# Kernel optimization log

Hardware: AMD Instinct MI355X
Metric: run time of the kernel (lower is better)

Reference implementation:

```python
import jax, jax.numpy as jnp
import numpy as np

B, T, D, H = 2, 1024, 1024, 16
HS = D // H
EPS = 1e-5
SCALE = float(np.sqrt(HS))  # faithful bug: scores / hs**(-0.5) == scores * sqrt(hs)


def setup_inputs() -> dict:
    key = jax.random.key(0)
    ks = jax.random.split(key, 20)
    n = lambda k, shape: jax.random.normal(k, shape, dtype=jnp.float32) * 0.02
    return {
        "src": jax.random.normal(ks[0], (B, T, D), dtype=jnp.float32),
        "att": jax.random.normal(ks[1], (B, T, D), dtype=jnp.float32),
        # causal masked self-attention (no biases on q/k/v)
        "wq_m": n(ks[2], (H, D, HS)), "wk_m": n(ks[3], (H, D, HS)), "wv_m": n(ks[4], (H, D, HS)),
        "proj_m_w": n(ks[5], (D, D)), "proj_m_b": jnp.zeros((D,), jnp.float32),
        # final (cross) attention (biases on q/k/v)
        "wq_f": n(ks[6], (H, D, HS)), "wk_f": n(ks[7], (H, D, HS)), "wv_f": n(ks[8], (H, D, HS)),
        "bq_f": jnp.zeros((H, HS), jnp.float32), "bk_f": jnp.zeros((H, HS), jnp.float32),
        "bv_f": jnp.zeros((H, HS), jnp.float32),
        "proj_f_w": n(ks[9], (D, D)), "proj_f_b": jnp.zeros((D,), jnp.float32),
        # FFN
        "w1": n(ks[10], (D, 4 * D)), "b1": jnp.zeros((4 * D,), jnp.float32),
        "w2": n(ks[11], (4 * D, D)), "b2": jnp.zeros((D,), jnp.float32),
        # shared RMSNorm weight (one instance reused at all three sites)
        "norm_w": jnp.ones((D,), jnp.float32),
    }


def rmsnorm(x, w):
    return x * jax.lax.rsqrt(jnp.mean(x * x, axis=-1, keepdims=True) + EPS) * w


def masked_attn(x, wq, wk, wv):
    q = jnp.einsum('btd,hde->bhte', x, wq)
    k = jnp.einsum('btd,hde->bhte', x, wk)
    v = jnp.einsum('btd,hde->bhte', x, wv)
    scores = jnp.einsum('bhte,bhse->bhts', q, k) * SCALE  # [B,H,T,T]
    causal = jnp.tril(jnp.ones((T, T), dtype=bool))
    scores = jnp.where(causal, scores, -jnp.inf)
    a = jax.nn.softmax(scores, axis=-1)
    o = jnp.einsum('bhts,bhse->bhte', a, v)
    return o.transpose(0, 2, 1, 3).reshape(B, T, D)  # concat heads


def final_attn(x, att, wq, bq, wk, bk, wv, bv):
    q = jnp.einsum('btd,hde->bhte', att, wq) + bq[None, :, None, :]
    k = jnp.einsum('btd,hde->bhte', att, wk) + bk[None, :, None, :]
    v = jnp.einsum('btd,hde->bhte', x, wv) + bv[None, :, None, :]
    scores = jnp.einsum('bhte,bhse->bhts', q, k) * SCALE
    a = jax.nn.softmax(scores, axis=-1)
    o = jnp.einsum('bhts,bhse->bhte', a, v)
    return o.transpose(0, 2, 1, 3).reshape(B, T, D)


def reference(src, att, wq_m, wk_m, wv_m, proj_m_w, proj_m_b,
              wq_f, wk_f, wv_f, bq_f, bk_f, bv_f, proj_f_w, proj_f_b,
              w1, b1, w2, b2, norm_w):
    # masked self-attention block
    m = masked_attn(rmsnorm(src, norm_w), wq_m, wk_m, wv_m)
    m_out = src + (m @ proj_m_w + proj_m_b)
    # cross attention block (q/k from norm(att), v from m_out)
    f = final_attn(m_out, rmsnorm(att, norm_w), wq_f, bq_f, wk_f, bk_f, wv_f, bv_f)
    f_out = m_out + (f @ proj_f_w + proj_f_b)
    # FFN block
    h = rmsnorm(f_out, norm_w)
    h = jax.nn.gelu(h @ w1 + b1, approximate=False) @ w2 + b2
    return f_out + h
```

## Files before the change

### kernel.cpp

```cpp
#include <hip/hip_runtime.h>
#include <math.h>

#define BB 2
#define TT 1024
#define DD 1024
#define HH 16
#define HS 64
#define NROWS (BB*TT)

typedef _Float16 f16;
typedef __attribute__((ext_vector_type(8))) _Float16 half8;
typedef __attribute__((ext_vector_type(4))) _Float16 half4;
typedef __attribute__((ext_vector_type(4))) float f32x4;

constexpr float EPS   = 1e-5f;
constexpr float SCALE = 8.0f;

__device__ __forceinline__ void load_lds16(const f16* g, f16* l) {
    __builtin_amdgcn_global_load_lds(
        (const __attribute__((address_space(1))) unsigned int*)g,
        (__attribute__((address_space(3))) unsigned int*)l, 16, 0, 0);
}

__device__ __forceinline__ int xcd_swizzle(int lin, int total) {
    if ((total & 7) == 0) {
        const int chunk = total >> 3;
        lin = (lin & 7) * chunk + (lin >> 3);
    }
    return lin;
}

__global__ __launch_bounds__(256) void rmsnorm_kernel(const float* __restrict__ x,
                                                      const float* __restrict__ w,
                                                      f16* __restrict__ out) {
    const int row = blockIdx.x;
    const int tid = threadIdx.x;
    const float* xr = x + (size_t)row * DD;

    float4 xv = reinterpret_cast<const float4*>(xr)[tid];
    float ss = xv.x*xv.x + xv.y*xv.y + xv.z*xv.z + xv.w*xv.w;

    __shared__ float red[256];
    red[tid] = ss; __syncthreads();
    for (int s = 128; s > 0; s >>= 1) {
        if (tid < s) red[tid] += red[tid + s];
        __syncthreads();
    }
    const float inv = rsqrtf(red[0] * (1.0f / DD) + EPS);

    float4 wv = reinterpret_cast<const float4*>(w)[tid];
    half4 o;
    o.x = (f16)(xv.x * inv * wv.x);
    o.y = (f16)(xv.y * inv * wv.y);
    o.z = (f16)(xv.z * inv * wv.z);
    o.w = (f16)(xv.w * inv * wv.w);
    *reinterpret_cast<half4*>(&out[(size_t)row * DD + tid * 4]) = o;
}

__global__ __launch_bounds__(256) void wtrans_all(
    const float* __restrict__ wq_m, const float* __restrict__ wk_m,
    const float* __restrict__ wv_m, const float* __restrict__ proj_m_w,
    const float* __restrict__ wq_f, const float* __restrict__ wk_f,
    const float* __restrict__ wv_f, const float* __restrict__ proj_f_w,
    const float* __restrict__ w1,   const float* __restrict__ w2,
    f16* __restrict__ d_qkvm, f16* __restrict__ d_projm,
    f16* __restrict__ d_qkvf, f16* __restrict__ d_projf,
    f16* __restrict__ d_w1,   f16* __restrict__ d_w2,
    const float* __restrict__ bq, const float* __restrict__ bk,
    const float* __restrict__ bv, float* __restrict__ biascat)
{
    const int bid = blockIdx.x;
    const int tid = threadIdx.x;
    const size_t M_ = 1024 * 1024;

    if (bid >= 4096) {
        #pragma unroll
        for (int r = 0; r < 4; ++r) {
            const int j = r * 256 + tid;
            biascat[j] = bq[j]; biascat[j + 1024] = bk[j]; biascat[j + 2048] = bv[j];
        }
        return;
    }

    const float* W; f16* Wt; int K, N, lognk, t; bool headw;
    if (bid < 768)       { const int m = bid >> 8;
                           W = (m == 0) ? wq_m : (m == 1) ? wk_m : wv_m;
                           Wt = d_qkvm + (size_t)m * M_;
                           K = 1024; N = 1024; lognk = 4; headw = true;  t = bid & 255; }
    else if (bid < 1024) { W = proj_m_w; Wt = d_projm;
                           K = 1024; N = 1024; lognk = 4; headw = false; t = bid - 768; }
    else if (bid < 1792) { const int m = (bid - 1024) >> 8;
                           W = (m == 0) ? wq_f : (m == 1) ? wk_f : wv_f;
                           Wt = d_qkvf + (size_t)m * M_;
                           K = 1024; N = 1024; lognk = 4; headw = true;  t = (bid - 1024) & 255; }
    else if (bid < 2048) { W = proj_f_w; Wt = d_projf;
                           K = 1024; N = 1024; lognk = 4; headw = false; t = bid - 1792; }
    else if (bid < 3072) { W = w1; Wt = d_w1;
                           K = 1024; N = 4096; lognk = 4; headw = false; t = bid - 2048; }
    else                 { W = w2; Wt = d_w2;
                           K = 4096; N = 1024; lognk = 6; headw = false; t = bid - 3072; }

    const int k0 = (t & ((1 << lognk) - 1)) * 64;
    const int n0 = (t >> lognk) * 64;

    __shared__ float tt[64][65];
    #pragma unroll
    for (int r = 0; r < 4; ++r) {
        const int idx = tid + r * 256;
        const int kl  = idx >> 4;
        const int nl4 = (idx & 15) * 4;
        const float* gp;
        if (headw) {
            gp = W + ((size_t)(n0 >> 6) * K + (k0 + kl)) * 64 + nl4;
        } else {
            gp = W + (size_t)(k0 + kl) * N + n0 + nl4;
        }
        float4 v = *reinterpret_cast<const float4*>(gp);
        tt[kl][nl4 + 0] = v.x; tt[kl][nl4 + 1] = v.y;
        tt[kl][nl4 + 2] = v.z; tt[kl][nl4 + 3] = v.w;
    }
    __syncthreads();
    #pragma unroll
    for (int r = 0; r < 4; ++r) {
        const int idx = tid + r * 256;
        const int nl  = idx >> 4;
        const int kl4 = (idx & 15) * 4;
        half4 o;
        o.x = (f16)tt[kl4 + 0][nl];
        o.y = (f16)tt[kl4 + 1][nl];
        o.z = (f16)tt[kl4 + 2][nl];
        o.w = (f16)tt[kl4 + 3][nl];
        *reinterpret_cast<half4*>(&Wt[(size_t)(n0 + nl) * K + k0 + kl4]) = o;
    }
}

template<int BM, int EPI, bool HEADOUT, bool SPLITA, bool OHALF, bool OUT2, bool PARTIAL>
__global__ __launch_bounds__(256, 2) void gemm_mfma(
    const f16* __restrict__ A1,
    const f16* __restrict__ A2,
    const f16* __restrict__ Bt,
    const float* __restrict__ bias,
    const float* __restrict__ resid,
    float* __restrict__ outF,
    f16* __restrict__ outH,
    f16* __restrict__ outH2,
    int N, int K, int splitN)
{
    constexpr int BK = 32;
    constexpr int MI = 4;
    constexpr int NI = (BM == 128) ? 4 : 2;
    constexpr int WN = (BM == 128) ? 64 : 32;
    constexpr int ASLOT = BM * 4;
    constexpr int AINST = ASLOT / 256;

    __shared__ f16 ldsA[2][ASLOT * 8];
    __shared__ f16 ldsB[2][512 * 8];

    const int tid  = threadIdx.x;
    const int lane = tid & 63;
    const int wid  = tid >> 6;
    const int gy = gridDim.y;
    const int lin = xcd_swizzle(blockIdx.y * gridDim.x + blockIdx.x,
                                gridDim.x * gy);
    const int m0 = (lin % gy) * BM;
    const int n0 = (lin / gy) * 128;
    const int wm = (BM == 128) ? (wid >> 1) : 0;
    const int wn = (BM == 128) ? (wid & 1) : wid;

    const int Klen  = K / gridDim.z;
    const int kbase = blockIdx.z * Klen;

    const f16* Aptr = (SPLITA && n0 >= splitN) ? A2 : A1;

    f32x4 acc[MI][NI];
    #pragma unroll
    for (int i = 0; i < MI; ++i)
        #pragma unroll
        for (int j = 0; j < NI; ++j)
            acc[i][j] = (f32x4){0.f, 0.f, 0.f, 0.f};

    auto stage = [&](int buf, int kt) {
        const int k0 = kbase + kt * BK;
        #pragma unroll
        for (int i = 0; i < AINST; ++i) {
            const int s   = (wid * AINST + i) * 64 + lane;
            const int kh  = s / BM;
            const int row = s % BM;
            load_lds16(Aptr + (size_t)(m0 + row) * K + (k0 + kh * 8),
                       &ldsA[buf][s * 8]);
        }
        #pragma unroll
        for (int i = 0; i < 2; ++i) {
            const int s   = (wid * 2 + i) * 64 + lane;
            const int kh  = s >> 7;
            const int col = s & 127;
            load_lds16(Bt + (size_t)(n0 + col) * K + (k0 + kh * 8),
                       &ldsB[buf][s * 8]);
        }
    };

    const int NT = Klen / BK;
    stage(0, 0);
    __syncthreads();
    int cur = 0;
    const int l15 = lane & 15, l4 = lane >> 4;
    for (int kt = 0; kt < NT; ++kt) {
        if (kt + 1 < NT) stage(cur ^ 1, kt + 1);
        half8 af[MI], bfr[NI];
        #pragma unroll
        for (int mi = 0; mi < MI; ++mi)
            af[mi] = *reinterpret_cast<const half8*>(
                &ldsA[cur][(l4 * BM + wm * 64 + mi * 16 + l15) * 8]);
        #pragma unroll
        for (int ni = 0; ni < NI; ++ni)
            bfr[ni] = *reinterpret_cast<const half8*>(
                &ldsB[cur][(l4 * 128 + wn * WN + ni * 16 + l15) * 8]);
        #pragma unroll
        for (int mi = 0; mi < MI; ++mi)
            #pragma unroll
            for (int ni = 0; ni < NI; ++ni)
                acc[mi][ni] = __builtin_amdgcn_mfma_f32_16x16x32_f16(
                    af[mi], bfr[ni], acc[mi][ni], 0, 0, 0);
        __syncthreads();
        cur ^= 1;
    }

    float* pout = nullptr;
    if (PARTIAL) {
        const size_t MN = (size_t)gridDim.y * BM * N;
        pout = outF + (size_t)blockIdx.z * MN;
    }

    #pragma unroll
    for (int mi = 0; mi < MI; ++mi) {
        #pragma unroll
        for (int ni = 0; ni < NI; ++ni) {
            #pragma unroll
            for (int r = 0; r < 4; ++r) {
                const int row = m0 + wm * 64 + mi * 16 + l4 * 4 + r;
                const int col = n0 + wn * WN + ni * 16 + l15;
                float v = acc[mi][ni][r];
                if (PARTIAL) {
                    pout[(size_t)row * N + col] = v;
                    continue;
                }
                if (EPI >= 1) v += bias[col];
                if (EPI == 2) v = 0.5f * v * (1.0f + erff(v * 0.70710678118f));
                if (EPI == 3) v += resid[(size_t)row * N + col];
                size_t oidx;
                if (HEADOUT) {
                    const int mat = col >> 10;
                    const int h = (col >> 6) & 15, e = col & 63;
                    const int b = row >> 10, t = row & (TT - 1);
                    oidx = (size_t)mat * ((size_t)NROWS * DD)
                         + ((size_t)((b * HH + h) * TT + t)) * HS + e;
                } else {
                    oidx = (size_t)row * N + col;
                }
                if (OHALF) outH[oidx] = (f16)v;
                else       outF[oidx] = v;
                if (OUT2)  outH2[oidx] = (f16)v;
            }
        }
    }
}

template<bool OUT2>
__global__ __launch_bounds__(256) void reduce4(const float* __restrict__ part,
                                               const float* __restrict__ bias,
                                               const float* __restrict__ resid,
                                               float* __restrict__ outF,
                                               f16* __restrict__ outH2,
                                               int N) {
    const size_t MN  = (size_t)gridDim.x * 1024;
    const size_t idx = ((size_t)blockIdx.x * 256 + threadIdx.x) * 4;
    float4 a = *reinterpret_cast<const float4*>(part + idx);
    float4 b = *reinterpret_cast<const float4*>(part + MN + idx);
    float4 c = *reinterpret_cast<const float4*>(part + 2 * MN + idx);
    float4 d = *reinterpret_cast<const float4*>(part + 3 * MN + idx);
    float4 bi = *reinterpret_cast<const float4*>(bias + (idx & (size_t)(N - 1)));
    float4 rs = *reinterpret_cast<const float4*>(resid + idx);
    float4 o;
    o.x = a.x + b.x + c.x + d.x + bi.x + rs.x;
    o.y = a.y + b.y + c.y + d.y + bi.y + rs.y;
    o.z = a.z + b.z + c.z + d.z + bi.z + rs.z;
    o.w = a.w + b.w + c.w + d.w + bi.w + rs.w;
    *reinterpret_cast<float4*>(outF + idx) = o;
    if (OUT2) {
        half4 h;
        h.x = (f16)o.x; h.y = (f16)o.y; h.z = (f16)o.z; h.w = (f16)o.w;
        *reinterpret_cast<half4*>(outH2 + idx) = h;
    }
}

template<bool CAUSAL>
__global__ __launch_bounds__(256) void attn_mfma(const f16* __restrict__ Q,
                                                 const f16* __restrict__ Kg,
                                                 const f16* __restrict__ Vg,
                                                 f16* __restrict__ O) {
    const int iq  = blockIdx.x;
    const int bh  = blockIdx.y;
    const int tid = threadIdx.x;
    const int lane = tid & 63;
    const int w   = tid >> 6;
    const int l15 = lane & 15, l4 = lane >> 4;

    __shared__ f16 Ks[512 * 8];
    __shared__ f16 VT[64 * 72];
    __shared__ f16 Ps[4][16 * 72];

    const f16* qb = Q  + ((size_t)bh * TT + (size_t)iq * 64) * HS;
    const f16* kb = Kg + (size_t)bh * TT * HS;
    const f16* vb = Vg + (size_t)bh * TT * HS;

    half8 qf[2];
    #pragma unroll
    for (int ks = 0; ks < 2; ++ks)
        qf[ks] = *reinterpret_cast<const half8*>(
            qb + (size_t)(w * 16 + l15) * HS + ks * 32 + l4 * 8);

    f32x4 oacc[4];
    #pragma unroll
    for (int ni = 0; ni < 4; ++ni) oacc[ni] = (f32x4){0.f, 0.f, 0.f, 0.f};
    float m_run[4], l_run[4];
    #pragma unroll
    for (int r = 0; r < 4; ++r) { m_run[r] = -1e30f; l_run[r] = 0.f; }

    const int sp  = lane & 31;
    const int ehv = lane >> 5;
    const int c0  = w * 16 + ehv * 8;

    const int ntiles = CAUSAL ? (iq + 1) : (TT / 64);
    for (int js = 0; js < ntiles; ++js) {
        __syncthreads();

        #pragma unroll
        for (int i = 0; i < 2; ++i) {
            const int slot = (w * 2 + i) * 64 + lane;
            load_lds16(kb + (size_t)(js * 64 + (slot & 63)) * HS + (slot >> 6) * 8,
                       &Ks[slot * 8]);
        }
        {
            const f16* vrow = vb + (size_t)(js * 64 + 2 * sp) * HS + c0;
            uint4 r0 = *reinterpret_cast<const uint4*>(vrow);
            uint4 r1 = *reinterpret_cast<const uint4*>(vrow + HS);
            const unsigned rc0[4] = {r0.x, r0.y, r0.z, r0.w};
            const unsigned rc1[4] = {r1.x, r1.y, r1.z, r1.w};
            #pragma unroll
            for (int i = 0; i < 8; ++i) {
                const unsigned lo = (i & 1) ? (rc0[i >> 1] >> 16) : (rc0[i >> 1] & 0xffffu);
                const unsigned hi = (i & 1) ? (rc1[i >> 1] >> 16) : (rc1[i >> 1] & 0xffffu);
                *reinterpret_cast<unsigned*>(&VT[(c0 + i) * 72 + 2 * sp]) = lo | (hi << 16);
            }
        }
        __syncthreads();

        f32x4 sacc[4];
        #pragma unroll
        for (int ni = 0; ni < 4; ++ni) sacc[ni] = (f32x4){0.f, 0.f, 0.f, 0.f};
        #pragma unroll
        for (int ks = 0; ks < 2; ++ks) {
            #pragma unroll
            for (int ni = 0; ni < 4; ++ni) {
                half8 kf = *reinterpret_cast<const half8*>(
                    &Ks[((ks * 4 + l4) * 64 + ni * 16 + l15) * 8]);
                sacc[ni] = __builtin_amdgcn_mfma_f32_16x16x32_f16(qf[ks], kf, sacc[ni], 0, 0, 0);
            }
        }

        float sv[4][4];
        #pragma unroll
        for (int ni = 0; ni < 4; ++ni) {
            #pragma unroll
            for (int r = 0; r < 4; ++r) {
                float x = sacc[ni][r] * SCALE;
                if (CAUSAL && js == iq) {
                    const int sg = js * 64 + ni * 16 + l15;
                    const int qg = iq * 64 + w * 16 + l4 * 4 + r;
                    if (sg > qg) x = -1e30f;
                }
                sv[ni][r] = x;
            }
        }

        #pragma unroll
        for (int r = 0; r < 4; ++r) {
            float rm = fmaxf(fmaxf(sv[0][r], sv[1][r]), fmaxf(sv[2][r], sv[3][r]));
            rm = fmaxf(rm, __shfl_xor(rm, 1));
            rm = fmaxf(rm, __shfl_xor(rm, 2));
            rm = fmaxf(rm, __shfl_xor(rm, 4));
            rm = fmaxf(rm, __shfl_xor(rm, 8));
            const float mnew = fmaxf(m_run[r], rm);
            const float corr = __expf(m_run[r] - mnew);
            float p0 = __expf(sv[0][r] - mnew);
            float p1 = __expf(sv[1][r] - mnew);
            float p2 = __expf(sv[2][r] - mnew);
            float p3 = __expf(sv[3][r] - mnew);
            float sum = p0 + p1 + p2 + p3;
            sum += __shfl_xor(sum, 1);
            sum += __shfl_xor(sum, 2);
            sum += __shfl_xor(sum, 4);
            sum += __shfl_xor(sum, 8);
            l_run[r] = l_run[r] * corr + sum;
            m_run[r] = mnew;
            #pragma unroll
            for (int ni = 0; ni < 4; ++ni) oacc[ni][r] *= corr;
            f16* prow = &Ps[w][(l4 * 4 + r) * 72];
            prow[ 0 + l15] = (f16)p0;
            prow[16 + l15] = (f16)p1;
            prow[32 + l15] = (f16)p2;
            prow[48 + l15] = (f16)p3;
        }

        #pragma unroll
        for (int ks = 0; ks < 2; ++ks) {
            half8 pf = *reinterpret_cast<const half8*>(&Ps[w][l15 * 72 + ks * 32 + l4 * 8]);
            #pragma unroll
            for (int ni = 0; ni < 4; ++ni) {
                half8 vf = *reinterpret_cast<const half8*>(
                    &VT[(ni * 16 + l15) * 72 + ks * 32 + l4 * 8]);
                oacc[ni] = __builtin_amdgcn_mfma_f32_16x16x32_f16(pf, vf, oacc[ni], 0, 0, 0);
            }
        }
    }

    const int b = bh >> 4, h = bh & (HH - 1);
    #pragma unroll
    for (int r = 0; r < 4; ++r) {
        const float inv = 1.0f / l_run[r];
        const int t = iq * 64 + w * 16 + l4 * 4 + r;
        #pragma unroll
        for (int ni = 0; ni < 4; ++ni)
            O[((size_t)(b * TT + t)) * DD + h * HS + ni * 16 + l15] =
                (f16)(oacc[ni][r] * inv);
    }
}

extern "C" void kernel_launch(void* const* d_in, const int* in_sizes, int n_in,
                              void* d_out, int out_size, void* d_ws, size_t ws_size,
                              hipStream_t stream) {
    const float* src      = (const float*)d_in[0];
    const float* att      = (const float*)d_in[1];
    const float* wq_m     = (const float*)d_in[2];
    const float* wk_m     = (const float*)d_in[3];
    const float* wv_m     = (const float*)d_in[4];
    const float* proj_m_w = (const float*)d_in[5];
    const float* proj_m_b = (const float*)d_in[6];
    const float* wq_f     = (const float*)d_in[7];
    const float* wk_f     = (const float*)d_in[8];
    const float* wv_f     = (const float*)d_in[9];
    const float* bq_f     = (const float*)d_in[10];
    const float* bk_f     = (const float*)d_in[11];
    const float* bv_f     = (const float*)d_in[12];
    const float* proj_f_w = (const float*)d_in[13];
    const float* proj_f_b = (const float*)d_in[14];
    const float* w1       = (const float*)d_in[15];
    const float* b1       = (const float*)d_in[16];
    const float* w2       = (const float*)d_in[17];
    const float* b2       = (const float*)d_in[18];
    const float* norm_w   = (const float*)d_in[19];

    const size_t M_ = 1024 * 1024;
    f16* wsb = (f16*)d_ws;
    f16* wt_qkvm = wsb;
    f16* wt_projm = wsb + 3 * M_;
    f16* wt_qkvf = wsb + 4 * M_;
    f16* wt_projf = wsb + 7 * M_;
    f16* wt_w1   = wsb + 8 * M_;
    f16* wt_w2   = wsb + 12 * M_;
    f16* xn  = wsb + 16 * M_;
    f16* qkv = wsb + 18 * M_;
    f16* ao  = wsb + 24 * M_;
    f16* h1  = wsb + 18 * M_;
    float* m_out = (float*)(wsb + 26 * M_);
    float* partb = (float*)(wsb + 30 * M_);
    f16* mo_h  = (f16*)d_out;
    float* biascat = (float*)((char*)d_out + 4 * 1024 * 1024);
    float* f_out = (float*)d_out;
    float* outp  = (float*)d_out;
    (void)ws_size; (void)in_sizes; (void)n_in;

    const dim3 blk(256);
    const int BIG = 1 << 30;
    const dim3 gQKV(24, 32);
    const dim3 gW1(32, 32);
    const dim3 gSPLIT(8, 32, 4);
    const dim3 gRED(2048);

    wtrans_all<<<dim3(4097), blk, 0, stream>>>(
        wq_m, wk_m, wv_m, proj_m_w, wq_f, wk_f, wv_f, proj_f_w, w1, w2,
        wt_qkvm, wt_projm, wt_qkvf, wt_projf, wt_w1, wt_w2,
        bq_f, bk_f, bv_f, biascat);

    rmsnorm_kernel<<<dim3(NROWS), blk, 0, stream>>>(src, norm_w, xn);
    gemm_mfma<64, 0, true, false, true, false, false><<<gQKV, blk, 0, stream>>>(
        xn, nullptr, wt_qkvm, nullptr, nullptr, nullptr, qkv, nullptr, 3072, 1024, BIG);
    attn_mfma<true><<<dim3(16, 32), blk, 0, stream>>>(qkv, qkv + 2 * M_, qkv + 4 * M_, ao);
    gemm_mfma<64, 0, false, false, false, false, true><<<gSPLIT, blk, 0, stream>>>(
        ao, nullptr, wt_projm, nullptr, nullptr, partb, nullptr, nullptr, 1024, 1024, BIG);
    reduce4<true><<<gRED, blk, 0, stream>>>(partb, proj_m_b, src, m_out, mo_h, 1024);

    rmsnorm_kernel<<<dim3(NROWS), blk, 0, stream>>>(att, norm_w, xn);
    gemm_mfma<64, 1, true, true, true, false, false><<<gQKV, blk, 0, stream>>>(
        xn, mo_h, wt_qkvf, biascat, nullptr, nullptr, qkv, nullptr, 3072, 1024, 2048);
    attn_mfma<false><<<dim3(16, 32), blk, 0, stream>>>(qkv, qkv + 2 * M_, qkv + 4 * M_, ao);
    gemm_mfma<64, 0, false, false, false, false, true><<<gSPLIT, blk, 0, stream>>>(
        ao, nullptr, wt_projf, nullptr, nullptr, partb, nullptr, nullptr, 1024, 1024, BIG);
    reduce4<false><<<gRED, blk, 0, stream>>>(partb, proj_f_b, m_out, f_out, nullptr, 1024);

    rmsnorm_kernel<<<dim3(NROWS), blk, 0, stream>>>(f_out, norm_w, xn);
    gemm_mfma<64, 2, false, false, true, false, false><<<gW1, blk, 0, stream>>>(
        xn, nullptr, wt_w1, b1, nullptr, nullptr, h1, nullptr, 4096, 1024, BIG);
    gemm_mfma<64, 0, false, false, false, false, true><<<gSPLIT, blk, 0, stream>>>(
        h1, nullptr, wt_w2, nullptr, nullptr, partb, nullptr, nullptr, 1024, 4096, BIG);
    reduce4<false><<<gRED, blk, 0, stream>>>(partb, b2, f_out, outp, nullptr, 1024);
}
```

Baseline: 364.5 us.

## Restructure pipeline: merge norms and QKV GEMMs, fp16 split-K partials, fused reduce-norm

Both RMSNorms (src and att) now run in one launch. The masked QKV and the cross-attention Q/K projections run as a single 5120-wide GEMM with BM=128, and only the V projection of m_out stays as a separate GEMM. Split-K partials are stored in fp16 instead of fp32, which halves partial-buffer traffic. The second reduction also fuses the final RMSNorm, which removes a launch. Risks are precision loss from the fp16 partials and the residual m_out now being kept only in fp16. BM=128 tiles may also reduce occupancy and CU fill for the smaller grids.

```diff
diff --git a/kernel.cpp b/kernel.cpp
--- a/kernel.cpp
+++ b/kernel.cpp
@@ -30,12 +30,16 @@
     return lin;
 }
 
-__global__ __launch_bounds__(256) void rmsnorm_kernel(const float* __restrict__ x,
-                                                      const float* __restrict__ w,
-                                                      f16* __restrict__ out) {
-    const int row = blockIdx.x;
+__global__ __launch_bounds__(256) void rms2_kernel(const float* __restrict__ src,
+                                                   const float* __restrict__ att,
+                                                   const float* __restrict__ w,
+                                                   f16* __restrict__ xn_s,
+                                                   f16* __restrict__ xn_a) {
+    const int bid = blockIdx.x;
     const int tid = threadIdx.x;
-    const float* xr = x + (size_t)row * DD;
+    const int row = bid & (NROWS - 1);
+    const float* xr = ((bid < NROWS) ? src : att) + (size_t)row * DD;
+    f16* out = ((bid < NROWS) ? xn_s : xn_a) + (size_t)row * DD;
 
     float4 xv = reinterpret_cast<const float4*>(xr)[tid];
     float ss = xv.x*xv.x + xv.y*xv.y + xv.z*xv.z + xv.w*xv.w;
@@ -54,7 +58,7 @@
     o.y = (f16)(xv.y * inv * wv.y);
     o.z = (f16)(xv.z * inv * wv.z);
     o.w = (f16)(xv.w * inv * wv.w);
-    *reinterpret_cast<half4*>(&out[(size_t)row * DD + tid * 4]) = o;
+    *reinterpret_cast<half4*>(&out[tid * 4]) = o;
 }
 
 __global__ __launch_bounds__(256) void wtrans_all(
@@ -63,41 +67,36 @@
     const float* __restrict__ wq_f, const float* __restrict__ wk_f,
     const float* __restrict__ wv_f, const float* __restrict__ proj_f_w,
     const float* __restrict__ w1,   const float* __restrict__ w2,
-    f16* __restrict__ d_qkvm, f16* __restrict__ d_projm,
-    f16* __restrict__ d_qkvf, f16* __restrict__ d_projf,
-    f16* __restrict__ d_w1,   f16* __restrict__ d_w2,
+    f16* __restrict__ wt,
     const float* __restrict__ bq, const float* __restrict__ bk,
-    const float* __restrict__ bv, float* __restrict__ biascat)
+    float* __restrict__ biascat)
 {
     const int bid = blockIdx.x;
     const int tid = threadIdx.x;
     const size_t M_ = 1024 * 1024;
 
     if (bid >= 4096) {
-        #pragma unroll
-        for (int r = 0; r < 4; ++r) {
-            const int j = r * 256 + tid;
-            biascat[j] = bq[j]; biascat[j + 1024] = bk[j]; biascat[j + 2048] = bv[j];
-        }
+        for (int j = tid; j < 5120; j += 256)
+            biascat[j] = (j < 3072) ? 0.f : ((j < 4096) ? bq[j - 3072] : bk[j - 4096]);
         return;
     }
 
     const float* W; f16* Wt; int K, N, lognk, t; bool headw;
     if (bid < 768)       { const int m = bid >> 8;
                            W = (m == 0) ? wq_m : (m == 1) ? wk_m : wv_m;
-                           Wt = d_qkvm + (size_t)m * M_;
+                           Wt = wt + (size_t)m * M_;
                            K = 1024; N = 1024; lognk = 4; headw = true;  t = bid & 255; }
-    else if (bid < 1024) { W = proj_m_w; Wt = d_projm;
+    else if (bid < 1024) { W = proj_m_w; Wt = wt + 6 * M_;
                            K = 1024; N = 1024; lognk = 4; headw = false; t = bid - 768; }
     else if (bid < 1792) { const int m = (bid - 1024) >> 8;
                            W = (m == 0) ? wq_f : (m == 1) ? wk_f : wv_f;
-                           Wt = d_qkvf + (size_t)m * M_;
+                           Wt = wt + (size_t)(3 + m) * M_;
                            K = 1024; N = 1024; lognk = 4; headw = true;  t = (bid - 1024) & 255; }
-    else if (bid < 2048) { W = proj_f_w; Wt = d_projf;
+    else if (bid < 2048) { W = proj_f_w; Wt = wt + 7 * M_;
                            K = 1024; N = 1024; lognk = 4; headw = false; t = bid - 1792; }
-    else if (bid < 3072) { W = w1; Wt = d_w1;
+    else if (bid < 3072) { W = w1; Wt = wt + 8 * M_;
                            K = 1024; N = 4096; lognk = 4; headw = false; t = bid - 2048; }
-    else                 { W = w2; Wt = d_w2;
+    else                 { W = w2; Wt = wt + 12 * M_;
                            K = 4096; N = 1024; lognk = 6; headw = false; t = bid - 3072; }
 
     const int k0 = (t & ((1 << lognk) - 1)) * 64;
@@ -134,16 +133,14 @@
     }
 }
 
-template<int BM, int EPI, bool HEADOUT, bool SPLITA, bool OHALF, bool OUT2, bool PARTIAL>
+template<int BM, int EPI, bool HEADOUT, bool SPLITA, bool OHALF, bool PARTIAL>
 __global__ __launch_bounds__(256, 2) void gemm_mfma(
     const f16* __restrict__ A1,
     const f16* __restrict__ A2,
     const f16* __restrict__ Bt,
     const float* __restrict__ bias,
-    const float* __restrict__ resid,
     float* __restrict__ outF,
     f16* __restrict__ outH,
-    f16* __restrict__ outH2,
     int N, int K, int splitN)
 {
     constexpr int BK = 32;
@@ -225,10 +222,10 @@
         cur ^= 1;
     }
 
-    float* pout = nullptr;
+    f16* pout = nullptr;
     if (PARTIAL) {
         const size_t MN = (size_t)gridDim.y * BM * N;
-        pout = outF + (size_t)blockIdx.z * MN;
+        pout = outH + (size_t)blockIdx.z * MN;
     }
 
     #pragma unroll
@@ -241,12 +238,11 @@
                 const int col = n0 + wn * WN + ni * 16 + l15;
                 float v = acc[mi][ni][r];
                 if (PARTIAL) {
-                    pout[(size_t)row * N + col] = v;
+                    pout[(size_t)row * N + col] = (f16)v;
                     continue;
                 }
                 if (EPI >= 1) v += bias[col];
                 if (EPI == 2) v = 0.5f * v * (1.0f + erff(v * 0.70710678118f));
-                if (EPI == 3) v += resid[(size_t)row * N + col];
                 size_t oidx;
                 if (HEADOUT) {
                     const int mat = col >> 10;
@@ -259,37 +255,69 @@
                 }
                 if (OHALF) outH[oidx] = (f16)v;
                 else       outF[oidx] = v;
-                if (OUT2)  outH2[oidx] = (f16)v;
             }
         }
     }
 }
 
-template<bool OUT2>
-__global__ __launch_bounds__(256) void reduce4(const float* __restrict__ part,
-                                               const float* __restrict__ bias,
-                                               const float* __restrict__ resid,
-                                               float* __restrict__ outF,
-                                               f16* __restrict__ outH2,
-                                               int N) {
-    const size_t MN  = (size_t)gridDim.x * 1024;
-    const size_t idx = ((size_t)blockIdx.x * 256 + threadIdx.x) * 4;
-    float4 a = *reinterpret_cast<const float4*>(part + idx);
-    float4 b = *reinterpret_cast<const float4*>(part + MN + idx);
-    float4 c = *reinterpret_cast<const float4*>(part + 2 * MN + idx);
-    float4 d = *reinterpret_cast<const float4*>(part + 3 * MN + idx);
-    float4 bi = *reinterpret_cast<const float4*>(bias + (idx & (size_t)(N - 1)));
-    float4 rs = *reinterpret_cast<const float4*>(resid + idx);
-    float4 o;
-    o.x = a.x + b.x + c.x + d.x + bi.x + rs.x;
-    o.y = a.y + b.y + c.y + d.y + bi.y + rs.y;
-    o.z = a.z + b.z + c.z + d.z + bi.z + rs.z;
-    o.w = a.w + b.w + c.w + d.w + bi.w + rs.w;
-    *reinterpret_cast<float4*>(outF + idx) = o;
-    if (OUT2) {
+template<int MODE>
+__global__ __launch_bounds__(256) void reduce_fuse(const f16* __restrict__ part,
+                                                   const float* __restrict__ bias,
+                                                   const float* __restrict__ residF,
+                                                   const f16* __restrict__ residH,
+                                                   float* __restrict__ outF,
+                                                   f16* __restrict__ outH,
+                                                   const float* __restrict__ normw,
+                                                   f16* __restrict__ xnout) {
+    const size_t MN  = (size_t)NROWS * 1024;
+    const int tid = threadIdx.x;
+    const size_t idx = ((size_t)blockIdx.x * 256 + tid) * 4;
+    float o[4];
+    {
+        half4 p0 = *reinterpret_cast<const half4*>(part + idx);
+        half4 p1 = *reinterpret_cast<const half4*>(part + MN + idx);
+        half4 p2 = *reinterpret_cast<const half4*>(part + 2 * MN + idx);
+        half4 p3 = *reinterpret_cast<const half4*>(part + 3 * MN + idx);
+        float4 bi = *reinterpret_cast<const float4*>(bias + (idx & 1023));
+        o[0] = (float)p0.x + (float)p1.x + (float)p2.x + (float)p3.x + bi.x;
+        o[1] = (float)p0.y + (float)p1.y + (float)p2.y + (float)p3.y + bi.y;
+        o[2] = (float)p0.z + (float)p1.z + (float)p2.z + (float)p3.z + bi.z;
+        o[3] = (float)p0.w + (float)p1.w + (float)p2.w + (float)p3.w + bi.w;
+    }
+    if (MODE == 0 || MODE == 2) {
+        float4 rs = *reinterpret_cast<const float4*>(residF + idx);
+        o[0] += rs.x; o[1] += rs.y; o[2] += rs.z; o[3] += rs.w;
+    } else {
+        half4 rh = *reinterpret_cast<const half4*>(residH + idx);
+        o[0] += (float)rh.x; o[1] += (float)rh.y; o[2] += (float)rh.z; o[3] += (float)rh.w;
+    }
+
+    if (MODE == 0) {
         half4 h;
-        h.x = (f16)o.x; h.y = (f16)o.y; h.z = (f16)o.z; h.w = (f16)o.w;
-        *reinterpret_cast<half4*>(outH2 + idx) = h;
+        h.x = (f16)o[0]; h.y = (f16)o[1]; h.z = (f16)o[2]; h.w = (f16)o[3];
+        *reinterpret_cast<half4*>(outH + idx) = h;
+        return;
+    }
+
+    float4 ov = {o[0], o[1], o[2], o[3]};
+    *reinterpret_cast<float4*>(outF + idx) = ov;
+
+    if (MODE == 1) {
+        __shared__ float red[256];
+        red[tid] = o[0]*o[0] + o[1]*o[1] + o[2]*o[2] + o[3]*o[3];
+        __syncthreads();
+        for (int s = 128; s > 0; s >>= 1) {
+            if (tid < s) red[tid] += red[tid + s];
+            __syncthreads();
+        }
+        const float inv = rsqrtf(red[0] * (1.0f / DD) + EPS);
+        float4 nw = *reinterpret_cast<const float4*>(normw + (idx & 1023));
+        half4 h;
+        h.x = (f16)(o[0] * inv * nw.x);
+        h.y = (f16)(o[1] * inv * nw.y);
+        h.z = (f16)(o[2] * inv * nw.z);
+        h.w = (f16)(o[3] * inv * nw.w);
+        *reinterpret_cast<half4*>(xnout + idx) = h;
     }
 }
 
@@ -462,56 +490,55 @@
 
     const size_t M_ = 1024 * 1024;
     f16* wsb = (f16*)d_ws;
-    f16* wt_qkvm = wsb;
-    f16* wt_projm = wsb + 3 * M_;
-    f16* wt_qkvf = wsb + 4 * M_;
-    f16* wt_projf = wsb + 7 * M_;
-    f16* wt_w1   = wsb + 8 * M_;
-    f16* wt_w2   = wsb + 12 * M_;
-    f16* xn  = wsb + 16 * M_;
-    f16* qkv = wsb + 18 * M_;
-    f16* ao  = wsb + 24 * M_;
-    f16* h1  = wsb + 18 * M_;
-    float* m_out = (float*)(wsb + 26 * M_);
-    float* partb = (float*)(wsb + 30 * M_);
-    f16* mo_h  = (f16*)d_out;
-    float* biascat = (float*)((char*)d_out + 4 * 1024 * 1024);
+    f16* wt      = wsb;
+    f16* headbuf = wsb + 16 * M_;
+    f16* h1      = wsb + 16 * M_;
+    f16* xn_s    = wsb + 28 * M_;
+    f16* xn_a    = wsb + 30 * M_;
+    f16* ao      = wsb + 32 * M_;
+    f16* mo_h    = wsb + 34 * M_;
+    f16* partH   = wsb + 36 * M_;
+    float* biascat = (float*)d_out;
     float* f_out = (float*)d_out;
     float* outp  = (float*)d_out;
     (void)ws_size; (void)in_sizes; (void)n_in;
 
     const dim3 blk(256);
     const int BIG = 1 << 30;
-    const dim3 gQKV(24, 32);
-    const dim3 gW1(32, 32);
-    const dim3 gSPLIT(8, 32, 4);
+    const dim3 gQKV(40, 16);
+    const dim3 gVF(8, 32);
+    const dim3 gW1(32, 16);
+    const dim3 gSPLIT(8, 16, 4);
     const dim3 gRED(2048);
 
     wtrans_all<<<dim3(4097), blk, 0, stream>>>(
         wq_m, wk_m, wv_m, proj_m_w, wq_f, wk_f, wv_f, proj_f_w, w1, w2,
-        wt_qkvm, wt_projm, wt_qkvf, wt_projf, wt_w1, wt_w2,
-        bq_f, bk_f, bv_f, biascat);
-
-    rmsnorm_kernel<<<dim3(NROWS), blk, 0, stream>>>(src, norm_w, xn);
-    gemm_mfma<64, 0, true, false, true, false, false><<<gQKV, blk, 0, stream>>>(
-        xn, nullptr, wt_qkvm, nullptr, nullptr, nullptr, qkv, nullptr, 3072, 1024, BIG);
-    attn_mfma<true><<<dim3(16, 32), blk, 0, stream>>>(qkv, qkv + 2 * M_, qkv + 4 * M_, ao);
-    gemm_mfma<64, 0, false, false, false, false, true><<<gSPLIT, blk, 0, stream>>>(
-        ao, nullptr, wt_projm, nullptr, nullptr, partb, nullptr, nullptr, 1024, 1024, BIG);
-    reduce4<true><<<gRED, blk, 0, stream>>>(partb, proj_m_b, src, m_out, mo_h, 1024);
-
-    rmsnorm_kernel<<<dim3(NROWS), blk, 0, stream>>>(att, norm_w, xn);
-    gemm_mfma<64, 1, true, true, true, false, false><<<gQKV, blk, 0, stream>>>(
-        xn, mo_h, wt_qkvf, biascat, nullptr, nullptr, qkv, nullptr, 3072, 1024, 2048);
-    attn_mfma<false><<<dim3(16, 32), blk, 0, stream>>>(qkv, qkv + 2 * M_, qkv + 4 * M_, ao);
-    gemm_mfma<64, 0, false, false, false, false, true><<<gSPLIT, blk, 0, stream>>>(
-        ao, nullptr, wt_projf, nullptr, nullptr, partb, nullptr, nullptr, 1024, 1024, BIG);
-    reduce4<false><<<gRED, blk, 0, stream>>>(partb, proj_f_b, m_out, f_out, nullptr, 1024);
-
-    rmsnorm_kernel<<<dim3(NROWS), blk, 0, stream>>>(f_out, norm_w, xn);
-    gemm_mfma<64, 2, false, false, true, false, false><<<gW1, blk, 0, stream>>>(
-        xn, nullptr, wt_w1, b1, nullptr, nullptr, h1, nullptr, 4096, 1024, BIG);
-    gemm_mfma<64, 0, false, false, false, false, true><<<gSPLIT, blk, 0, stream>>>(
-        h1, nullptr, wt_w2, nullptr, nullptr, partb, nullptr, nullptr, 1024, 4096, BIG);
-    reduce4<false><<<gRED, blk, 0, stream>>>(partb, b2, f_out, outp, nullptr, 1024);
-}
+        wt, bq_f, bk_f, biascat);
+    rms2_kernel<<<dim3(2 * NROWS), blk, 0, stream>>>(src, att, norm_w, xn_s, xn_a);
+
+    gemm_mfma<128, 1, true, true, true, false><<<gQKV, blk, 0, stream>>>(
+        xn_s, xn_a, wt, biascat, nullptr, headbuf, 5120, 1024, 3072);
+
+    attn_mfma<true><<<dim3(16, 32), blk, 0, stream>>>(
+        headbuf, headbuf + 2 * M_, headbuf + 4 * M_, ao);
+    gemm_mfma<128, 0, false, false, false, true><<<gSPLIT, blk, 0, stream>>>(
+        ao, nullptr, wt + 6 * M_, nullptr, nullptr, partH, 1024, 1024, BIG);
+    reduce_fuse<0><<<gRED, blk, 0, stream>>>(
+        partH, proj_m_b, src, nullptr, nullptr, mo_h, nullptr, nullptr);
+
+    gemm_mfma<64, 1, true, false, true, false><<<gVF, blk, 0, stream>>>(
+        mo_h, nullptr, wt + 5 * M_, bv_f, nullptr, headbuf + 10 * M_, 1024, 1024, BIG);
+    attn_mfma<false><<<dim3(16, 32), blk, 0, stream>>>(
+        headbuf + 6 * M_, headbuf + 8 * M_, headbuf + 10 * M_, ao);
+    gemm_mfma<128, 0, false, false, false, true><<<gSPLIT, blk, 0, stream>>>(
+        ao, nullptr, wt + 7 * M_, nullptr, nullptr, partH, 1024, 1024, BIG);
+    reduce_fuse<1><<<gRED, blk, 0, stream>>>(
+        partH, proj_f_b, nullptr, mo_h, f_out, nullptr, norm_w, xn_s);
+
+    gemm_mfma<128, 2, false, false, true, false><<<gW1, blk, 0, stream>>>(
+        xn_s, nullptr, wt + 8 * M_, b1, nullptr, h1, 4096, 1024, BIG);
+    gemm_mfma<128, 0, false, false, false, true><<<gSPLIT, blk, 0, stream>>>(
+        h1, nullptr, wt + 12 * M_, nullptr, nullptr, partH, 1024, 4096, BIG);
+    reduce_fuse<2><<<gRED, blk, 0, stream>>>(
+        partH, b2, f_out, nullptr, outp, nullptr, nullptr, nullptr);
+}
```

Result: faster. 312.2 us (-14.3%).
